# Performance work log

Hardware: AMD Instinct MI355X
Metric: run time of the kernel (lower is better)

## Reference

```python
import jax, jax.numpy as jnp
import numpy as np

BIT_WIDTH = 8
UP = float(2 ** (BIT_WIDTH - 1) - 1)   # 127
LOW = float(-(2 ** (BIT_WIDTH - 1)))   # -128


def setup_inputs() -> dict:
    key = jax.random.key(0)
    k1, k2, k3, k4, k5 = jax.random.split(key, 5)
    B, Cin, H, W = 32, 256, 56, 56
    Cout, kH, kW = 256, 3, 3
    x = jax.random.normal(k1, (B, Cin, H, W), dtype=jnp.float32)
    weight = jax.random.normal(k2, (Cout, Cin, kH, kW), dtype=jnp.float32) * 0.05
    bias = jax.random.normal(k3, (Cout,), dtype=jnp.float32) * 0.1
    # positive quantization scales (roughly map |w|~0.15, |x|~3 into int8 range)
    sw = jax.random.uniform(k4, (Cout,), minval=200.0, maxval=800.0, dtype=jnp.float32)
    sx = jax.random.uniform(k5, (1,), minval=20.0, maxval=40.0, dtype=jnp.float32)
    return {"x": x, "weight": weight, "bias": bias, "sw": sw, "sx": sx}


def reference(x, weight, bias, sw, sx):
    """QConv2d forward in q_inference (quant-simulation) mode:
    per-out-channel fake-quantize weight, per-tensor fake-quantize input,
    then float conv2d + bias. jnp.round matches torch.round (half-to-even)."""
    swb = sw[:, None, None, None]                      # [Cout,1,1,1]
    q_w = jnp.round(jnp.clip(weight * swb, LOW, UP)) / swb
    q_x = jnp.round(jnp.clip(x * sx[0], LOW, UP)) / sx[0]
    out = jax.lax.conv_general_dilated(
        q_x, q_w,
        window_strides=(1, 1),
        padding=((1, 1), (1, 1)),
        dimension_numbers=("NCHW", "OIHW", "NCHW"),
    )
    return out + bias[None, :, None, None]
```

## Files before the change

kernel.cpp:

```cpp
#include <hip/hip_runtime.h>
#include <stdint.h>

typedef int int32x4 __attribute__((ext_vector_type(4)));

#define HW_        3136
#define CHW_       802816
#define HP_        58
#define WP_        58
#define PLANE_PIX  107648ull
#define PLANE_B    (PLANE_PIX*16)
#define QXP_BYTES  (16ull*PLANE_B)
#define QWT_BYTES  (9ull*16*256*16)

__device__ __forceinline__ signed char quant8(float v, float s) {
    float t = v * s;
    t = fmaxf(t, -128.0f);
    t = fminf(t, 127.0f);
    return (signed char)(int)rintf(t);
}

__global__ __launch_bounds__(256) void halo_zero_kernel(signed char* __restrict__ qxp2) {
    const int b = blockIdx.x, hp = blockIdx.y, tid = threadIdx.x;
    const int32x4 z = {0,0,0,0};
    const size_t rowpix = (size_t)(b*HP_ + hp)*WP_;
    if (hp == 0 || hp == HP_-1) {
        for (int q = tid; q < 16*WP_; q += 256) {
            int cq = q / WP_, wp = q - cq*WP_;
            *(int32x4*)(qxp2 + (cq*PLANE_PIX + rowpix + wp)*16) = z;
        }
    } else if (tid < 32) {
        int cq = tid >> 1, wp = (tid & 1) * (WP_-1);
        *(int32x4*)(qxp2 + (cq*PLANE_PIX + rowpix + wp)*16) = z;
    }
}

__global__ __launch_bounds__(256) void quant_w_kernel(
    const float* __restrict__ wgt, const float* __restrict__ sw,
    signed char* __restrict__ qwT2)
{
    __shared__ __align__(16) signed char lw[9*272];
    const int o = blockIdx.x, c = threadIdx.x;
    const float s = sw[o];
    const float* wp = wgt + ((size_t)o*256 + c)*9;
    #pragma unroll
    for (int kk = 0; kk < 9; ++kk)
        lw[kk*272 + c] = quant8(wp[kk], s);
    __syncthreads();
    if (c < 144) {
        int kk = c / 16, cq = c - kk*16;
        int32x4 v = *(const int32x4*)&lw[kk*272 + cq*16];
        *(int32x4*)(qwT2 + ((size_t)(kk*16 + cq)*256 + o)*16) = v;
    }
}

__global__ __launch_bounds__(256) void quant_x_kernel(
    const float* __restrict__ x, const float* __restrict__ sx,
    signed char* __restrict__ qxp2)
{
    __shared__ __align__(16) signed char tile[56*272];
    const int tid = threadIdx.x;
    const int bh = blockIdx.x;
    const int b = bh / 56, h = bh % 56;
    const float s = sx[0];
    const size_t xbase = (size_t)b*CHW_ + (size_t)h*56;
    #pragma unroll
    for (int it = 0; it < 14; ++it) {
        int v = tid + it*256;
        int c = v / 14;
        int j = v - c*14;
        float4 f = *(const float4*)(x + xbase + (size_t)c*HW_ + 4*j);
        tile[(4*j+0)*272 + c] = quant8(f.x, s);
        tile[(4*j+1)*272 + c] = quant8(f.y, s);
        tile[(4*j+2)*272 + c] = quant8(f.z, s);
        tile[(4*j+3)*272 + c] = quant8(f.w, s);
    }
    __syncthreads();
    const size_t pbase = (size_t)(b*HP_ + h + 1)*WP_ + 1;
    #pragma unroll
    for (int it = 0; it < 4; ++it) {
        int q = tid + it*256;
        if (q < 896) {
            int cq = q / 56, w = q - cq*56;
            int32x4 v = *(const int32x4*)&tile[w*272 + cq*16];
            *(int32x4*)(qxp2 + (cq*PLANE_PIX + pbase + w)*16) = v;
        }
    }
}

__device__ __forceinline__ void load16_lds(const void* g, void* l) {
    __builtin_amdgcn_global_load_lds(
        (const unsigned int*)g,
        reinterpret_cast<__attribute__((address_space(3))) unsigned int*>(
            reinterpret_cast<uintptr_t>(l)),
        16, 0, 0);
}

__global__ __launch_bounds__(256, 4) void conv_kernel(
    const signed char* __restrict__ qxp2, const signed char* __restrict__ qwT2,
    const float* __restrict__ sw, const float* __restrict__ bias,
    const float* __restrict__ sx, float* __restrict__ out)
{
    __shared__ __align__(16) signed char ldsA[16384];
    __shared__ __align__(16) signed char ldsB[16384];
    __shared__ float invS[128];
    __shared__ float biasS[128];

    const int tid  = threadIdx.x;
    const int wave = tid >> 6;
    const int lane = tid & 63;
    const int quad = lane >> 4;
    const int l15  = lane & 15;
    const int s0 = blockIdx.x * 128;
    const int o0 = blockIdx.y * 128;

    if (tid < 128) {
        float s = sw[o0 + tid];
        invS[tid]  = 1.0f / (s * sx[0]);
        biasS[tid] = bias[o0 + tid];
    }

    const unsigned sp0 = (unsigned)(s0 + lane);
    const unsigned sp1 = (unsigned)(s0 + 64 + lane);
    unsigned b0 = sp0 / HW_, r0 = sp0 - b0*HW_;
    unsigned b1 = sp1 / HW_, r1 = sp1 - b1*HW_;
    unsigned h0 = r0 / 56,   w0 = r0 - h0*56;
    unsigned h1 = r1 / 56,   w1 = r1 - h1*56;
    const size_t bOff0 = ((size_t)(b0*HP_ + h0)*WP_ + w0)*16;
    const size_t bOff1 = ((size_t)(b1*HP_ + h1)*WP_ + w1)*16;
    const size_t aOff0 = (size_t)(o0 + lane)*16;
    const size_t aOff1 = aOff0 + 1024;

    int32x4 acc[4][4];
    #pragma unroll
    for (int i = 0; i < 4; ++i)
        #pragma unroll
        for (int j = 0; j < 4; ++j)
            acc[i][j] = (int32x4){0,0,0,0};

    const int wo = (wave & 1) << 6;
    const int wn = (wave >> 1) << 6;

    for (int kk = 0; kk < 9; ++kk) {
        const size_t kshift = (size_t)((kk/3)*WP_ + (kk%3))*16;
        const size_t aKK = (size_t)kk*16*4096;
        #pragma unroll
        for (int hf = 0; hf < 2; ++hf) {
            const int cq0 = hf*8;
            #pragma unroll
            for (int t = 0; t < 2; ++t) {
                const int kc = 2*wave + t;
                const int cq = cq0 + kc;
                const signed char* aG = qwT2 + aKK + (size_t)cq*4096;
                load16_lds(aG + aOff0, ldsA + kc*2048);
                load16_lds(aG + aOff1, ldsA + kc*2048 + 1024);
                const signed char* bG = qxp2 + (size_t)cq*PLANE_B + kshift;
                load16_lds(bG + bOff0, ldsB + kc*2048);
                load16_lds(bG + bOff1, ldsB + kc*2048 + 1024);
            }
            __syncthreads();
            #pragma unroll
            for (int ks = 0; ks < 2; ++ks) {
                const int ck = (ks*4 + quad)*2048;
                int32x4 af[4], bf[4];
                #pragma unroll
                for (int t = 0; t < 4; ++t) {
                    af[t] = *(const int32x4*)&ldsA[ck + (wo + t*16 + l15)*16];
                    bf[t] = *(const int32x4*)&ldsB[ck + (wn + t*16 + l15)*16];
                }
                #pragma unroll
                for (int mt = 0; mt < 4; ++mt)
                    #pragma unroll
                    for (int nt = 0; nt < 4; ++nt)
                        acc[mt][nt] = __builtin_amdgcn_mfma_i32_16x16x64_i8(
                            af[mt], bf[nt], acc[mt][nt], 0, 0, 0);
            }
            __syncthreads();
        }
    }

    #pragma unroll
    for (int nt = 0; nt < 4; ++nt) {
        unsigned sp = (unsigned)(s0 + wn + nt*16 + l15);
        unsigned b  = sp / HW_;
        unsigned pos = sp - b*HW_;
        float* outN = out + (size_t)b*CHW_ + pos + (size_t)o0*HW_;
        #pragma unroll
        for (int mt = 0; mt < 4; ++mt) {
            const int ob = wo + (mt << 4) + (quad << 2);
            #pragma unroll
            for (int r = 0; r < 4; ++r) {
                const int ol = ob + r;
                outN[(size_t)ol * HW_] = fmaf((float)acc[mt][nt][r], invS[ol], biasS[ol]);
            }
        }
    }
}

extern "C" void kernel_launch(void* const* d_in, const int* in_sizes, int n_in,
                              void* d_out, int out_size, void* d_ws, size_t ws_size,
                              hipStream_t stream)
{
    (void)in_sizes; (void)n_in; (void)out_size; (void)ws_size;
    const float* x    = (const float*)d_in[0];
    const float* wgt  = (const float*)d_in[1];
    const float* bias = (const float*)d_in[2];
    const float* sw   = (const float*)d_in[3];
    const float* sx   = (const float*)d_in[4];
    float* out = (float*)d_out;

    signed char* qxp2 = (signed char*)d_ws;
    signed char* qwT2 = qxp2 + QXP_BYTES;

    halo_zero_kernel<<<dim3(32, 58), 256, 0, stream>>>(qxp2);
    quant_w_kernel<<<256, 256, 0, stream>>>(wgt, sw, qwT2);
    quant_x_kernel<<<1792, 256, 0, stream>>>(x, sx, qxp2);
    conv_kernel<<<dim3(784, 2), 256, 0, stream>>>(qxp2, qwT2, sw, bias, sx, out);
}
```

Baseline: 304.9 us.

## Stage conv epilogue through LDS for float4 stores and simplify quant/halo kernels

```diff
diff --git a/kernel.cpp b/kernel.cpp
--- a/kernel.cpp
+++ b/kernel.cpp
@@ -19,18 +19,17 @@
     return (signed char)(int)rintf(t);
 }
 
-__global__ __launch_bounds__(256) void halo_zero_kernel(signed char* __restrict__ qxp2) {
-    const int b = blockIdx.x, hp = blockIdx.y, tid = threadIdx.x;
-    const int32x4 z = {0,0,0,0};
-    const size_t rowpix = (size_t)(b*HP_ + hp)*WP_;
-    if (hp == 0 || hp == HP_-1) {
-        for (int q = tid; q < 16*WP_; q += 256) {
-            int cq = q / WP_, wp = q - cq*WP_;
-            *(int32x4*)(qxp2 + (cq*PLANE_PIX + rowpix + wp)*16) = z;
-        }
-    } else if (tid < 32) {
-        int cq = tid >> 1, wp = (tid & 1) * (WP_-1);
-        *(int32x4*)(qxp2 + (cq*PLANE_PIX + rowpix + wp)*16) = z;
+__global__ __launch_bounds__(256) void halo_rows_kernel(signed char* __restrict__ qxp2) {
+    int idx = blockIdx.x*256 + threadIdx.x;
+    if (idx < 16*32*2*58) {
+        int cq = idx / (32*2*58);
+        int r  = idx % (32*2*58);
+        int b  = r / (2*58);
+        int t  = r % (2*58);
+        int hp = (t / 58) * (HP_-1);
+        int wp = t % 58;
+        *(int32x4*)(qxp2 + ((size_t)cq*PLANE_PIX + (size_t)(b*HP_+hp)*WP_ + wp)*16)
+            = (int32x4){0,0,0,0};
     }
 }
 
@@ -57,33 +56,35 @@
     const float* __restrict__ x, const float* __restrict__ sx,
     signed char* __restrict__ qxp2)
 {
-    __shared__ __align__(16) signed char tile[56*272];
     const int tid = threadIdx.x;
     const int bh = blockIdx.x;
     const int b = bh / 56, h = bh % 56;
     const float s = sx[0];
-    const size_t xbase = (size_t)b*CHW_ + (size_t)h*56;
-    #pragma unroll
-    for (int it = 0; it < 14; ++it) {
-        int v = tid + it*256;
-        int c = v / 14;
-        int j = v - c*14;
-        float4 f = *(const float4*)(x + xbase + (size_t)c*HW_ + 4*j);
-        tile[(4*j+0)*272 + c] = quant8(f.x, s);
-        tile[(4*j+1)*272 + c] = quant8(f.y, s);
-        tile[(4*j+2)*272 + c] = quant8(f.z, s);
-        tile[(4*j+3)*272 + c] = quant8(f.w, s);
-    }
-    __syncthreads();
-    const size_t pbase = (size_t)(b*HP_ + h + 1)*WP_ + 1;
-    #pragma unroll
-    for (int it = 0; it < 4; ++it) {
-        int q = tid + it*256;
-        if (q < 896) {
-            int cq = q / 56, w = q - cq*56;
-            int32x4 v = *(const int32x4*)&tile[w*272 + cq*16];
-            *(int32x4*)(qxp2 + (cq*PLANE_PIX + pbase + w)*16) = v;
-        }
+    if (tid < 224) {
+        const int w  = tid % 56;
+        const int cg = tid / 56;
+        const size_t xrow = (size_t)b*CHW_ + (size_t)h*56 + w;
+        const size_t pb = ((size_t)(b*HP_ + h + 1)*WP_ + 1 + w)*16;
+        #pragma unroll
+        for (int k = 0; k < 4; ++k) {
+            const int cq = cg*4 + k;
+            const float* xp = x + xrow + (size_t)(cq*16)*HW_;
+            int pk[4];
+            #pragma unroll
+            for (int g = 0; g < 4; ++g) {
+                int b0 = (unsigned char)quant8(xp[(size_t)(4*g+0)*HW_], s);
+                int b1 = (unsigned char)quant8(xp[(size_t)(4*g+1)*HW_], s);
+                int b2 = (unsigned char)quant8(xp[(size_t)(4*g+2)*HW_], s);
+                int b3 = (unsigned char)quant8(xp[(size_t)(4*g+3)*HW_], s);
+                pk[g] = b0 | (b1 << 8) | (b2 << 16) | (b3 << 24);
+            }
+            *(int32x4*)(qxp2 + (size_t)cq*PLANE_B + pb) = (int32x4){pk[0],pk[1],pk[2],pk[3]};
+        }
+    } else {
+        int t2 = tid - 224;
+        int cq = t2 >> 1, wp = (t2 & 1) * (WP_-1);
+        const size_t rowpix = (size_t)(b*HP_ + h + 1)*WP_;
+        *(int32x4*)(qxp2 + ((size_t)cq*PLANE_PIX + rowpix + wp)*16) = (int32x4){0,0,0,0};
     }
 }
 
@@ -100,10 +101,11 @@
     const float* __restrict__ sw, const float* __restrict__ bias,
     const float* __restrict__ sx, float* __restrict__ out)
 {
-    __shared__ __align__(16) signed char ldsA[16384];
-    __shared__ __align__(16) signed char ldsB[16384];
+    __shared__ __align__(16) signed char smem[33792];
     __shared__ float invS[128];
     __shared__ float biasS[128];
+    signed char* ldsA = smem;
+    signed char* ldsB = smem + 16384;
 
     const int tid  = threadIdx.x;
     const int wave = tid >> 6;
@@ -178,20 +180,36 @@
         }
     }
 
+    float* lt = (float*)smem;
     #pragma unroll
-    for (int nt = 0; nt < 4; ++nt) {
-        unsigned sp = (unsigned)(s0 + wn + nt*16 + l15);
-        unsigned b  = sp / HW_;
-        unsigned pos = sp - b*HW_;
-        float* outN = out + (size_t)b*CHW_ + pos + (size_t)o0*HW_;
-        #pragma unroll
-        for (int mt = 0; mt < 4; ++mt) {
-            const int ob = wo + (mt << 4) + (quad << 2);
-            #pragma unroll
-            for (int r = 0; r < 4; ++r) {
-                const int ol = ob + r;
-                outN[(size_t)ol * HW_] = fmaf((float)acc[mt][nt][r], invS[ol], biasS[ol]);
-            }
+    for (int p = 0; p < 2; ++p) {
+        __syncthreads();
+        if ((wave & 1) == p) {
+            #pragma unroll
+            for (int mt = 0; mt < 4; ++mt)
+                #pragma unroll
+                for (int nt = 0; nt < 4; ++nt)
+                    #pragma unroll
+                    for (int r = 0; r < 4; ++r)
+                        lt[(mt*16 + quad*4 + r)*132 + wn + nt*16 + l15]
+                            = (float)acc[mt][nt][r];
+        }
+        __syncthreads();
+        #pragma unroll
+        for (int i = 0; i < 8; ++i) {
+            int idx = i*256 + tid;
+            int o = idx >> 5;
+            int c = idx & 31;
+            float4 v = *(const float4*)&lt[o*132 + 4*c];
+            int ol = p*64 + o;
+            float is = invS[ol], bs = biasS[ol];
+            unsigned sp = (unsigned)(s0 + 4*c);
+            unsigned b  = sp / HW_;
+            unsigned pos = sp - b*HW_;
+            float4 wv;
+            wv.x = fmaf(v.x, is, bs); wv.y = fmaf(v.y, is, bs);
+            wv.z = fmaf(v.z, is, bs); wv.w = fmaf(v.w, is, bs);
+            *(float4*)(out + (size_t)b*CHW_ + (size_t)(o0 + ol)*HW_ + pos) = wv;
         }
     }
 }
@@ -211,7 +229,7 @@
     signed char* qxp2 = (signed char*)d_ws;
     signed char* qwT2 = qxp2 + QXP_BYTES;
 
-    halo_zero_kernel<<<dim3(32, 58), 256, 0, stream>>>(qxp2);
+    halo_rows_kernel<<<232, 256, 0, stream>>>(qxp2);
     quant_w_kernel<<<256, 256, 0, stream>>>(wgt, sw, qwT2);
     quant_x_kernel<<<1792, 256, 0, stream>>>(x, sx, qxp2);
     conv_kernel<<<dim3(784, 2), 256, 0, stream>>>(qxp2, qwT2, sw, bias, sx, out);
```

Result: faster. 282.9 us (-7.2%).
